# Kernel tuning notes

Measured on AMD Instinct MI355X. Metric: run time of the kernel, lower is better.

The kernel has to match this reference:

```python
import jax, jax.numpy as jnp
import numpy as np

BS = 512          # number of nodes (batch)
EMBED = 256       # embed_dim
NHEAD = 8
HDIM = EMBED // NHEAD
E = BS * BS       # fully-connected intra-batch graph


def _xavier(key, shape):
    lim = float(np.sqrt(6.0 / (shape[0] + shape[1])))
    return jax.random.uniform(key, shape, jnp.float32, -lim, lim)


def setup_inputs() -> dict:
    key = jax.random.key(0)
    ks = jax.random.split(key, 6)
    feats = jax.random.normal(ks[0], (BS, EMBED), jnp.float32)
    # edges sorted by destination c, exactly BS edges per destination
    dst = jnp.repeat(jnp.arange(BS), BS)   # c
    src = jnp.tile(jnp.arange(BS), BS)     # r
    edge_index = jnp.stack([src, dst], axis=1).astype(jnp.int32)  # [E, 2], cols (r, c)
    edge_attr = jnp.zeros((E, 1), jnp.float32)  # unused by forward
    return {
        "feats": feats,
        "edge_index": edge_index,
        "edge_attr": edge_attr,
        "Wq": _xavier(ks[1], (EMBED, EMBED)), "bq": jnp.zeros((EMBED,), jnp.float32),
        "Wk": _xavier(ks[2], (EMBED, EMBED)), "bk": jnp.zeros((EMBED,), jnp.float32),
        "Wv": _xavier(ks[3], (EMBED, EMBED)), "bv": jnp.zeros((EMBED,), jnp.float32),
        "Wo": _xavier(ks[4], (EMBED, EMBED)), "bo": jnp.zeros((EMBED,), jnp.float32),
    }


def reference(feats, edge_index, edge_attr, Wq, bq, Wk, bk, Wv, bv, Wo, bo):
    bs = feats.shape[0]
    scale = 1.0 / np.sqrt(HDIM)
    # QKV projections (torch Linear: x @ W.T + b), split heads -> [h, n, d]
    q = (feats @ Wq.T + bq).reshape(bs, NHEAD, HDIM).transpose(1, 0, 2)
    k = (feats @ Wk.T + bk).reshape(bs, NHEAD, HDIM).transpose(1, 0, 2)
    v = (feats @ Wv.T + bv).reshape(bs, NHEAD, HDIM).transpose(1, 0, 2)
    r, c = edge_index[:, 0], edge_index[:, 1]
    qe = q[:, c, :]   # [h, E, d] query of destination node
    ke = k[:, r, :]   # [h, E, d] key of source node
    ve = v[:, r, :]   # [h, E, d] value of source node
    sim = jnp.einsum('hed,hed->eh', qe, ke) * scale   # [E, h]
    # deterministic segment softmax over edges grouped by destination c
    m = jax.ops.segment_max(sim, c, num_segments=bs)  # [n, h]
    p = jnp.exp(sim - m[c])
    s = jax.ops.segment_sum(p, c, num_segments=bs)    # [n, h]
    attn = p / s[c]                                    # [E, h]
    # weight values and scatter-add per destination (aggr='add')
    out_e = attn.T[..., None] * ve                     # [h, E, d]
    out_e = out_e.transpose(1, 0, 2).reshape(-1, NHEAD * HDIM)  # [E, h*d]
    agg = jax.ops.segment_sum(out_e, c, num_segments=bs)        # [n, embed]
    return agg @ Wo.T + bo
```

## Files before the change

kernel.cpp:

```cpp
#include <hip/hip_runtime.h>

#define BS 512
#define EMBED 256
#define NHEAD 8
#define HDIM 32

typedef __attribute__((ext_vector_type(8))) short short8;
typedef __attribute__((ext_vector_type(4))) float f32x4;

__device__ inline f32x4 mfma16(short8 a, short8 b, f32x4 c) {
    return __builtin_amdgcn_mfma_f32_16x16x32_bf16(a, b, c, 0, 0, 0);
}

__device__ inline unsigned short f2bf(float x) {
    unsigned int u = __float_as_uint(x);
    u += 0x7FFFu + ((u >> 16) & 1u);
    return (unsigned short)(u >> 16);
}
__device__ inline float bf2f(unsigned short h) {
    return __uint_as_float(((unsigned int)h) << 16);
}
__device__ inline void split8(const float* p, short8& hi, short8& lo) {
    float4 a = *(const float4*)p;
    float4 b = *(const float4*)(p + 4);
    float x[8] = {a.x, a.y, a.z, a.w, b.x, b.y, b.z, b.w};
#pragma unroll
    for (int j = 0; j < 8; ++j) {
        unsigned short h = f2bf(x[j]);
        hi[j] = (short)h;
        lo[j] = (short)f2bf(x[j] - bf2f(h));
    }
}

__global__ __launch_bounds__(256) void qkv_fused(
    const float* __restrict__ feats,
    const float* __restrict__ Wq, const float* __restrict__ Wk,
    const float* __restrict__ Wv,
    const float* __restrict__ bq, const float* __restrict__ bk,
    const float* __restrict__ bv,
    unsigned short* __restrict__ Qhi, unsigned short* __restrict__ Qlo,
    unsigned short* __restrict__ Khi, unsigned short* __restrict__ Klo,
    unsigned short* __restrict__ Vthi, unsigned short* __restrict__ Vtlo,
    float* __restrict__ OUT)
{
    const int gidx = blockIdx.x * 256 + threadIdx.x;
    if (gidx < 32768) {
        float4 z = {0.f, 0.f, 0.f, 0.f};
        ((float4*)OUT)[gidx] = z;
    }

    const int wave = blockIdx.x * 4 + (threadIdx.x >> 6);
    const int l = threadIdx.x & 63;
    const int r = l & 15, g = l >> 4;
    const int nt = wave % 48, mt = wave / 48;
    const int m0 = mt * 16, n0 = nt * 16;
    const int seg = n0 >> 8;
    const int nn = n0 & 255;
    const float* W = (seg == 0) ? Wq : (seg == 1) ? Wk : Wv;
    const float* bias = (seg == 0) ? bq : (seg == 1) ? bk : bv;

    const float* arow = feats + (m0 + r) * EMBED;
    const float* brow = W + (nn + r) * EMBED;

    f32x4 acc = {0.f, 0.f, 0.f, 0.f};
#pragma unroll
    for (int kb = 0; kb < 8; ++kb) {
        const int k0 = kb * 32 + g * 8;
        short8 ah, al, bh, bl;
        split8(arow + k0, ah, al);
        split8(brow + k0, bh, bl);
        acc = mfma16(ah, bh, acc);
        acc = mfma16(ah, bl, acc);
        acc = mfma16(al, bh, acc);
    }
    const float bb = bias[nn + r];

    if (seg < 2) {
        unsigned short* Dhi = seg ? Khi : Qhi;
        unsigned short* Dlo = seg ? Klo : Qlo;
#pragma unroll
        for (int r4 = 0; r4 < 4; ++r4) {
            const int i = m0 + g * 4 + r4;
            const int c = nn + r;
            float v = acc[r4] + bb;
            unsigned short hh = f2bf(v);
            Dhi[i * EMBED + c] = hh;
            Dlo[i * EMBED + c] = f2bf(v - bf2f(hh));
        }
    } else {
        const int c = nn + r;
        const int i0 = m0 + g * 4;
        ushort4 ph, pl;
        float v0 = acc[0] + bb, v1 = acc[1] + bb;
        float v2 = acc[2] + bb, v3 = acc[3] + bb;
        ph.x = f2bf(v0); ph.y = f2bf(v1); ph.z = f2bf(v2); ph.w = f2bf(v3);
        pl.x = f2bf(v0 - bf2f(ph.x)); pl.y = f2bf(v1 - bf2f(ph.y));
        pl.z = f2bf(v2 - bf2f(ph.z)); pl.w = f2bf(v3 - bf2f(ph.w));
        *(ushort4*)(Vthi + c * BS + i0) = ph;
        *(ushort4*)(Vtlo + c * BS + i0) = pl;
    }
}

__global__ __launch_bounds__(512) void attn_out(
    const unsigned short* __restrict__ Qhi, const unsigned short* __restrict__ Qlo,
    const unsigned short* __restrict__ Khi, const unsigned short* __restrict__ Klo,
    const unsigned short* __restrict__ Vthi, const unsigned short* __restrict__ Vtlo,
    const float* __restrict__ Wo, const float* __restrict__ bo,
    float* __restrict__ OUT)
{
    const int qt = blockIdx.x >> 3;
    const int h = blockIdx.x & 7;
    const int q0 = qt * 16;
    const int tid = threadIdx.x;
    const int w = tid >> 6, l = tid & 63;
    const int r = l & 15, g = l >> 4;

    __shared__ unsigned short Psm[16 * 512];
    __shared__ float Opart[8][2][256];
    __shared__ float Rpart[8][16];
    __shared__ float Agg[16][36];
    char* Pb = (char*)Psm;

    const short8 qhi = *(const short8*)(Qhi + (q0 + r) * EMBED + h * HDIM + g * 8);
    const short8 qlo = *(const short8*)(Qlo + (q0 + r) * EMBED + h * HDIM + g * 8);

    const float cs = 0.17677669529663687f;
    float rs[4] = {0.f, 0.f, 0.f, 0.f};

#pragma unroll
    for (int kt = 0; kt < 4; ++kt) {
        const int krow = w * 64 + kt * 16 + r;
        short8 kh = *(const short8*)(Khi + krow * EMBED + h * HDIM + g * 8);
        short8 kl = *(const short8*)(Klo + krow * EMBED + h * HDIM + g * 8);
        f32x4 acc = {0.f, 0.f, 0.f, 0.f};
        acc = mfma16(qhi, kh, acc);
        acc = mfma16(qhi, kl, acc);
        acc = mfma16(qlo, kh, acc);
#pragma unroll
        for (int r4 = 0; r4 < 4; ++r4) {
            float p = __expf(acc[r4] * cs);
            rs[r4] += p;
            const int q = g * 4 + r4;
            const int bofs = q * 1024 + ((krow * 2) ^ ((q & 7) << 4));
            *(unsigned short*)(Pb + bofs) = f2bf(p);
        }
    }
#pragma unroll
    for (int off = 1; off < 16; off <<= 1) {
#pragma unroll
        for (int r4 = 0; r4 < 4; ++r4) rs[r4] += __shfl_xor(rs[r4], off);
    }
    if (r == 0) {
#pragma unroll
        for (int r4 = 0; r4 < 4; ++r4) Rpart[w][g * 4 + r4] = rs[r4];
    }

    f32x4 o0 = {0.f, 0.f, 0.f, 0.f}, o1 = {0.f, 0.f, 0.f, 0.f};
    const unsigned short* V0h = Vthi + (h * HDIM + r) * BS;
    const unsigned short* V0l = Vtlo + (h * HDIM + r) * BS;
    const unsigned short* V1h = V0h + 16 * BS;
    const unsigned short* V1l = V0l + 16 * BS;
#pragma unroll
    for (int kc = 0; kc < 2; ++kc) {
        const int kb = w * 64 + kc * 32 + g * 8;
        const int bofs = r * 1024 + ((kb * 2) ^ ((r & 7) << 4));
        short8 pa = *(const short8*)(Pb + bofs);
        o0 = mfma16(pa, *(const short8*)(V0h + kb), o0);
        o0 = mfma16(pa, *(const short8*)(V0l + kb), o0);
        o1 = mfma16(pa, *(const short8*)(V1h + kb), o1);
        o1 = mfma16(pa, *(const short8*)(V1l + kb), o1);
    }
    ((f32x4*)&Opart[w][0][0])[l] = o0;
    ((f32x4*)&Opart[w][1][0])[l] = o1;
    __syncthreads();

    if (w < 2) {
        f32x4 o = ((f32x4*)&Opart[0][w][0])[l];
#pragma unroll
        for (int p = 1; p < 8; ++p) {
            f32x4 t = ((f32x4*)&Opart[p][w][0])[l];
            o[0] += t[0]; o[1] += t[1]; o[2] += t[2]; o[3] += t[3];
        }
#pragma unroll
        for (int r4 = 0; r4 < 4; ++r4) {
            const int q = g * 4 + r4;
            float rt = Rpart[0][q];
#pragma unroll
            for (int p = 1; p < 8; ++p) rt += Rpart[p][q];
            Agg[q][w * 16 + r] = o[r4] / rt;
        }
    }
    __syncthreads();

    short8 ah, al;
    split8(&Agg[r][g * 8], ah, al);
#pragma unroll
    for (int nsub = 0; nsub < 2; ++nsub) {
        const int j0 = w * 32 + nsub * 16;
        short8 bh, bl;
        split8(Wo + (j0 + r) * EMBED + h * HDIM + g * 8, bh, bl);
        f32x4 a = {0.f, 0.f, 0.f, 0.f};
        a = mfma16(ah, bh, a);
        a = mfma16(ah, bl, a);
        a = mfma16(al, bh, a);
#pragma unroll
        for (int r4 = 0; r4 < 4; ++r4) {
            const int row = q0 + g * 4 + r4;
            const int col = j0 + r;
            float v = a[r4];
            if (h == 0) v += bo[col];
            atomicAdd(&OUT[row * EMBED + col], v);
        }
    }
}

extern "C" void kernel_launch(void* const* d_in, const int* in_sizes, int n_in,
                              void* d_out, int out_size, void* d_ws, size_t ws_size,
                              hipStream_t stream) {
    const float* feats = (const float*)d_in[0];
    const float* Wq = (const float*)d_in[3];
    const float* bq = (const float*)d_in[4];
    const float* Wk = (const float*)d_in[5];
    const float* bk = (const float*)d_in[6];
    const float* Wv = (const float*)d_in[7];
    const float* bv = (const float*)d_in[8];
    const float* Wo = (const float*)d_in[9];
    const float* bo = (const float*)d_in[10];
    float* out = (float*)d_out;

    unsigned short* ws = (unsigned short*)d_ws;
    const size_t NE = (size_t)BS * EMBED;
    unsigned short* Qhi  = ws;
    unsigned short* Qlo  = Qhi + NE;
    unsigned short* Khi  = Qlo + NE;
    unsigned short* Klo  = Khi + NE;
    unsigned short* Vthi = Klo + NE;
    unsigned short* Vtlo = Vthi + NE;

    qkv_fused<<<384, 256, 0, stream>>>(feats, Wq, Wk, Wv, bq, bk, bv,
                                       Qhi, Qlo, Khi, Klo, Vthi, Vtlo, out);
    attn_out<<<256, 512, 0, stream>>>(Qhi, Qlo, Khi, Klo, Vthi, Vtlo,
                                      Wo, bo, out);
}
```

Baseline: 26.15 us.

## Give each block all heads per query tile, dropping atomics and output zeroing

The attention kernel now gives each block a 16-query tile. Each wave owns one head and streams all 512 keys in 64-key chunks, so the softmax sum and P·V stay in registers. The 16×256 aggregate is then projected through Wo inside the block and written directly, which removes the atomicAdd reduction and the output-zeroing pass. Wo is pre-split into bf16 hi/lo once in the QKV kernel, and that kernel uses 32×32 wave tiles for more operand reuse. The cost is far fewer blocks (32 attention, 96 QKV), which leaves most compute units idle and lengthens the serial work per wave.

```diff
diff --git a/kernel.cpp b/kernel.cpp
--- a/kernel.cpp
+++ b/kernel.cpp
@@ -35,69 +35,94 @@
 __global__ __launch_bounds__(256) void qkv_fused(
     const float* __restrict__ feats,
     const float* __restrict__ Wq, const float* __restrict__ Wk,
-    const float* __restrict__ Wv,
+    const float* __restrict__ Wv, const float* __restrict__ Wo,
     const float* __restrict__ bq, const float* __restrict__ bk,
     const float* __restrict__ bv,
     unsigned short* __restrict__ Qhi, unsigned short* __restrict__ Qlo,
     unsigned short* __restrict__ Khi, unsigned short* __restrict__ Klo,
     unsigned short* __restrict__ Vthi, unsigned short* __restrict__ Vtlo,
-    float* __restrict__ OUT)
+    unsigned short* __restrict__ Wohi, unsigned short* __restrict__ Wolo)
 {
     const int gidx = blockIdx.x * 256 + threadIdx.x;
-    if (gidx < 32768) {
-        float4 z = {0.f, 0.f, 0.f, 0.f};
-        ((float4*)OUT)[gidx] = z;
+    if (gidx < 16384) {
+        float4 v = ((const float4*)Wo)[gidx];
+        ushort4 ph, pl;
+        ph.x = f2bf(v.x); pl.x = f2bf(v.x - bf2f(ph.x));
+        ph.y = f2bf(v.y); pl.y = f2bf(v.y - bf2f(ph.y));
+        ph.z = f2bf(v.z); pl.z = f2bf(v.z - bf2f(ph.z));
+        ph.w = f2bf(v.w); pl.w = f2bf(v.w - bf2f(ph.w));
+        ((ushort4*)Wohi)[gidx] = ph;
+        ((ushort4*)Wolo)[gidx] = pl;
     }
 
     const int wave = blockIdx.x * 4 + (threadIdx.x >> 6);
     const int l = threadIdx.x & 63;
     const int r = l & 15, g = l >> 4;
-    const int nt = wave % 48, mt = wave / 48;
-    const int m0 = mt * 16, n0 = nt * 16;
+    const int nt = wave % 24, mt = wave / 24;
+    const int m0 = mt * 32, n0 = nt * 32;
     const int seg = n0 >> 8;
     const int nn = n0 & 255;
     const float* W = (seg == 0) ? Wq : (seg == 1) ? Wk : Wv;
     const float* bias = (seg == 0) ? bq : (seg == 1) ? bk : bv;
 
-    const float* arow = feats + (m0 + r) * EMBED;
-    const float* brow = W + (nn + r) * EMBED;
-
-    f32x4 acc = {0.f, 0.f, 0.f, 0.f};
+    const float* a0 = feats + (m0 + r) * EMBED;
+    const float* a1 = a0 + 16 * EMBED;
+    const float* b0 = W + (nn + r) * EMBED;
+    const float* b1 = b0 + 16 * EMBED;
+
+    f32x4 acc00 = {0,0,0,0}, acc01 = {0,0,0,0}, acc10 = {0,0,0,0}, acc11 = {0,0,0,0};
 #pragma unroll
     for (int kb = 0; kb < 8; ++kb) {
         const int k0 = kb * 32 + g * 8;
-        short8 ah, al, bh, bl;
-        split8(arow + k0, ah, al);
-        split8(brow + k0, bh, bl);
-        acc = mfma16(ah, bh, acc);
-        acc = mfma16(ah, bl, acc);
-        acc = mfma16(al, bh, acc);
-    }
-    const float bb = bias[nn + r];
-
-    if (seg < 2) {
-        unsigned short* Dhi = seg ? Khi : Qhi;
-        unsigned short* Dlo = seg ? Klo : Qlo;
-#pragma unroll
-        for (int r4 = 0; r4 < 4; ++r4) {
-            const int i = m0 + g * 4 + r4;
-            const int c = nn + r;
-            float v = acc[r4] + bb;
-            unsigned short hh = f2bf(v);
-            Dhi[i * EMBED + c] = hh;
-            Dlo[i * EMBED + c] = f2bf(v - bf2f(hh));
-        }
-    } else {
-        const int c = nn + r;
-        const int i0 = m0 + g * 4;
-        ushort4 ph, pl;
-        float v0 = acc[0] + bb, v1 = acc[1] + bb;
-        float v2 = acc[2] + bb, v3 = acc[3] + bb;
-        ph.x = f2bf(v0); ph.y = f2bf(v1); ph.z = f2bf(v2); ph.w = f2bf(v3);
-        pl.x = f2bf(v0 - bf2f(ph.x)); pl.y = f2bf(v1 - bf2f(ph.y));
-        pl.z = f2bf(v2 - bf2f(ph.z)); pl.w = f2bf(v3 - bf2f(ph.w));
-        *(ushort4*)(Vthi + c * BS + i0) = ph;
-        *(ushort4*)(Vtlo + c * BS + i0) = pl;
+        short8 A0h, A0l, A1h, A1l, B0h, B0l, B1h, B1l;
+        split8(a0 + k0, A0h, A0l);
+        split8(a1 + k0, A1h, A1l);
+        split8(b0 + k0, B0h, B0l);
+        split8(b1 + k0, B1h, B1l);
+        acc00 = mfma16(A0h, B0h, acc00);
+        acc01 = mfma16(A0h, B1h, acc01);
+        acc10 = mfma16(A1h, B0h, acc10);
+        acc11 = mfma16(A1h, B1h, acc11);
+        acc00 = mfma16(A0h, B0l, acc00);
+        acc01 = mfma16(A0h, B1l, acc01);
+        acc10 = mfma16(A1h, B0l, acc10);
+        acc11 = mfma16(A1h, B1l, acc11);
+        acc00 = mfma16(A0l, B0h, acc00);
+        acc01 = mfma16(A0l, B1h, acc01);
+        acc10 = mfma16(A1l, B0h, acc10);
+        acc11 = mfma16(A1l, B1h, acc11);
+    }
+
+#pragma unroll
+    for (int ti = 0; ti < 2; ++ti) {
+#pragma unroll
+        for (int tj = 0; tj < 2; ++tj) {
+            f32x4 a = (ti == 0) ? (tj == 0 ? acc00 : acc01)
+                                : (tj == 0 ? acc10 : acc11);
+            const int cn = nn + tj * 16 + r;
+            const float bb = bias[cn];
+            if (seg < 2) {
+                unsigned short* Dhi = seg ? Khi : Qhi;
+                unsigned short* Dlo = seg ? Klo : Qlo;
+#pragma unroll
+                for (int r4 = 0; r4 < 4; ++r4) {
+                    const int i = m0 + ti * 16 + g * 4 + r4;
+                    float v = a[r4] + bb;
+                    unsigned short hh = f2bf(v);
+                    Dhi[i * EMBED + cn] = hh;
+                    Dlo[i * EMBED + cn] = f2bf(v - bf2f(hh));
+                }
+            } else {
+                const int i0 = m0 + ti * 16 + g * 4;
+                ushort4 ph, pl;
+                float v0 = a[0] + bb, v1 = a[1] + bb, v2 = a[2] + bb, v3 = a[3] + bb;
+                ph.x = f2bf(v0); ph.y = f2bf(v1); ph.z = f2bf(v2); ph.w = f2bf(v3);
+                pl.x = f2bf(v0 - bf2f(ph.x)); pl.y = f2bf(v1 - bf2f(ph.y));
+                pl.z = f2bf(v2 - bf2f(ph.z)); pl.w = f2bf(v3 - bf2f(ph.w));
+                *(ushort4*)(Vthi + cn * BS + i0) = ph;
+                *(ushort4*)(Vtlo + cn * BS + i0) = pl;
+            }
+        }
     }
 }
 
@@ -105,111 +130,108 @@
     const unsigned short* __restrict__ Qhi, const unsigned short* __restrict__ Qlo,
     const unsigned short* __restrict__ Khi, const unsigned short* __restrict__ Klo,
     const unsigned short* __restrict__ Vthi, const unsigned short* __restrict__ Vtlo,
-    const float* __restrict__ Wo, const float* __restrict__ bo,
-    float* __restrict__ OUT)
+    const unsigned short* __restrict__ Wohi, const unsigned short* __restrict__ Wolo,
+    const float* __restrict__ bo, float* __restrict__ OUT)
 {
-    const int qt = blockIdx.x >> 3;
-    const int h = blockIdx.x & 7;
-    const int q0 = qt * 16;
+    const int q0 = blockIdx.x * 16;
     const int tid = threadIdx.x;
     const int w = tid >> 6, l = tid & 63;
     const int r = l & 15, g = l >> 4;
 
-    __shared__ unsigned short Psm[16 * 512];
-    __shared__ float Opart[8][2][256];
-    __shared__ float Rpart[8][16];
-    __shared__ float Agg[16][36];
-    char* Pb = (char*)Psm;
-
-    const short8 qhi = *(const short8*)(Qhi + (q0 + r) * EMBED + h * HDIM + g * 8);
-    const short8 qlo = *(const short8*)(Qlo + (q0 + r) * EMBED + h * HDIM + g * 8);
+    __shared__ unsigned short Psm[8][16 * 64];
+    __shared__ float Agg[16][260];
+    char* Pb = (char*)&Psm[w][0];
+
+    const short8 qhi = *(const short8*)(Qhi + (q0 + r) * EMBED + w * HDIM + g * 8);
+    const short8 qlo = *(const short8*)(Qlo + (q0 + r) * EMBED + w * HDIM + g * 8);
 
     const float cs = 0.17677669529663687f;
     float rs[4] = {0.f, 0.f, 0.f, 0.f};
-
-#pragma unroll
-    for (int kt = 0; kt < 4; ++kt) {
-        const int krow = w * 64 + kt * 16 + r;
-        short8 kh = *(const short8*)(Khi + krow * EMBED + h * HDIM + g * 8);
-        short8 kl = *(const short8*)(Klo + krow * EMBED + h * HDIM + g * 8);
-        f32x4 acc = {0.f, 0.f, 0.f, 0.f};
-        acc = mfma16(qhi, kh, acc);
-        acc = mfma16(qhi, kl, acc);
-        acc = mfma16(qlo, kh, acc);
-#pragma unroll
-        for (int r4 = 0; r4 < 4; ++r4) {
-            float p = __expf(acc[r4] * cs);
-            rs[r4] += p;
-            const int q = g * 4 + r4;
-            const int bofs = q * 1024 + ((krow * 2) ^ ((q & 7) << 4));
-            *(unsigned short*)(Pb + bofs) = f2bf(p);
-        }
-    }
-#pragma unroll
-    for (int off = 1; off < 16; off <<= 1) {
-#pragma unroll
-        for (int r4 = 0; r4 < 4; ++r4) rs[r4] += __shfl_xor(rs[r4], off);
-    }
-    if (r == 0) {
-#pragma unroll
-        for (int r4 = 0; r4 < 4; ++r4) Rpart[w][g * 4 + r4] = rs[r4];
-    }
-
     f32x4 o0 = {0.f, 0.f, 0.f, 0.f}, o1 = {0.f, 0.f, 0.f, 0.f};
-    const unsigned short* V0h = Vthi + (h * HDIM + r) * BS;
-    const unsigned short* V0l = Vtlo + (h * HDIM + r) * BS;
+
+    const unsigned short* V0h = Vthi + (w * HDIM + r) * BS;
+    const unsigned short* V0l = Vtlo + (w * HDIM + r) * BS;
     const unsigned short* V1h = V0h + 16 * BS;
     const unsigned short* V1l = V0l + 16 * BS;
-#pragma unroll
-    for (int kc = 0; kc < 2; ++kc) {
-        const int kb = w * 64 + kc * 32 + g * 8;
-        const int bofs = r * 1024 + ((kb * 2) ^ ((r & 7) << 4));
-        short8 pa = *(const short8*)(Pb + bofs);
-        o0 = mfma16(pa, *(const short8*)(V0h + kb), o0);
-        o0 = mfma16(pa, *(const short8*)(V0l + kb), o0);
-        o1 = mfma16(pa, *(const short8*)(V1h + kb), o1);
-        o1 = mfma16(pa, *(const short8*)(V1l + kb), o1);
-    }
-    ((f32x4*)&Opart[w][0][0])[l] = o0;
-    ((f32x4*)&Opart[w][1][0])[l] = o1;
+
+#pragma unroll
+    for (int t = 0; t < 8; ++t) {
+        const int t0 = t * 64;
+#pragma unroll
+        for (int kt = 0; kt < 4; ++kt) {
+            const int krow = t0 + kt * 16 + r;
+            short8 kh = *(const short8*)(Khi + krow * EMBED + w * HDIM + g * 8);
+            short8 kl = *(const short8*)(Klo + krow * EMBED + w * HDIM + g * 8);
+            f32x4 acc = {0.f, 0.f, 0.f, 0.f};
+            acc = mfma16(qhi, kh, acc);
+            acc = mfma16(qhi, kl, acc);
+            acc = mfma16(qlo, kh, acc);
+#pragma unroll
+            for (int r4 = 0; r4 < 4; ++r4) {
+                float p = __expf(acc[r4] * cs);
+                rs[r4] += p;
+                const int q = g * 4 + r4;
+                const int kk = kt * 16 + r;
+                const int bofs = q * 128 + ((kk * 2) ^ ((q & 7) << 4));
+                *(unsigned short*)(Pb + bofs) = f2bf(p);
+            }
+        }
+#pragma unroll
+        for (int kc = 0; kc < 2; ++kc) {
+            const int kk = kc * 32 + g * 8;
+            const int kb = t0 + kk;
+            const int bofs = r * 128 + ((kk * 2) ^ ((r & 7) << 4));
+            short8 pa = *(const short8*)(Pb + bofs);
+            o0 = mfma16(pa, *(const short8*)(V0h + kb), o0);
+            o0 = mfma16(pa, *(const short8*)(V0l + kb), o0);
+            o1 = mfma16(pa, *(const short8*)(V1h + kb), o1);
+            o1 = mfma16(pa, *(const short8*)(V1l + kb), o1);
+        }
+    }
+#pragma unroll
+    for (int off = 1; off < 16; off <<= 1) {
+#pragma unroll
+        for (int r4 = 0; r4 < 4; ++r4) rs[r4] += __shfl_xor(rs[r4], off);
+    }
+#pragma unroll
+    for (int r4 = 0; r4 < 4; ++r4) {
+        const int q = g * 4 + r4;
+        const float inv = 1.0f / rs[r4];
+        Agg[q][w * 32 + r] = o0[r4] * inv;
+        Agg[q][w * 32 + 16 + r] = o1[r4] * inv;
+    }
     __syncthreads();
 
-    if (w < 2) {
-        f32x4 o = ((f32x4*)&Opart[0][w][0])[l];
-#pragma unroll
-        for (int p = 1; p < 8; ++p) {
-            f32x4 t = ((f32x4*)&Opart[p][w][0])[l];
-            o[0] += t[0]; o[1] += t[1]; o[2] += t[2]; o[3] += t[3];
-        }
+    f32x4 p0 = {0.f, 0.f, 0.f, 0.f}, p1 = {0.f, 0.f, 0.f, 0.f};
+#pragma unroll
+    for (int kb = 0; kb < 8; ++kb) {
+        short8 ah, al;
+        split8(&Agg[r][kb * 32 + g * 8], ah, al);
+        {
+            const int j0 = w * 32;
+            short8 bh = *(const short8*)(Wohi + (j0 + r) * EMBED + kb * 32 + g * 8);
+            short8 bl = *(const short8*)(Wolo + (j0 + r) * EMBED + kb * 32 + g * 8);
+            p0 = mfma16(ah, bh, p0);
+            p0 = mfma16(ah, bl, p0);
+            p0 = mfma16(al, bh, p0);
+        }
+        {
+            const int j0 = w * 32 + 16;
+            short8 bh = *(const short8*)(Wohi + (j0 + r) * EMBED + kb * 32 + g * 8);
+            short8 bl = *(const short8*)(Wolo + (j0 + r) * EMBED + kb * 32 + g * 8);
+            p1 = mfma16(ah, bh, p1);
+            p1 = mfma16(ah, bl, p1);
+            p1 = mfma16(al, bh, p1);
+        }
+    }
+#pragma unroll
+    for (int nsub = 0; nsub < 2; ++nsub) {
+        const f32x4 a = nsub ? p1 : p0;
+        const int j0 = w * 32 + nsub * 16;
+        const float bb = bo[j0 + r];
 #pragma unroll
         for (int r4 = 0; r4 < 4; ++r4) {
-            const int q = g * 4 + r4;
-            float rt = Rpart[0][q];
-#pragma unroll
-            for (int p = 1; p < 8; ++p) rt += Rpart[p][q];
-            Agg[q][w * 16 + r] = o[r4] / rt;
-        }
-    }
-    __syncthreads();
-
-    short8 ah, al;
-    split8(&Agg[r][g * 8], ah, al);
-#pragma unroll
-    for (int nsub = 0; nsub < 2; ++nsub) {
-        const int j0 = w * 32 + nsub * 16;
-        short8 bh, bl;
-        split8(Wo + (j0 + r) * EMBED + h * HDIM + g * 8, bh, bl);
-        f32x4 a = {0.f, 0.f, 0.f, 0.f};
-        a = mfma16(ah, bh, a);
-        a = mfma16(ah, bl, a);
-        a = mfma16(al, bh, a);
-#pragma unroll
-        for (int r4 = 0; r4 < 4; ++r4) {
-            const int row = q0 + g * 4 + r4;
-            const int col = j0 + r;
-            float v = a[r4];
-            if (h == 0) v += bo[col];
-            atomicAdd(&OUT[row * EMBED + col], v);
+            OUT[(q0 + g * 4 + r4) * EMBED + j0 + r] = a[r4] + bb;
         }
     }
 }
@@ -230,15 +252,19 @@
 
     unsigned short* ws = (unsigned short*)d_ws;
     const size_t NE = (size_t)BS * EMBED;
+    const size_t WO = (size_t)EMBED * EMBED;
     unsigned short* Qhi  = ws;
     unsigned short* Qlo  = Qhi + NE;
     unsigned short* Khi  = Qlo + NE;
     unsigned short* Klo  = Khi + NE;
     unsigned short* Vthi = Klo + NE;
     unsigned short* Vtlo = Vthi + NE;
-
-    qkv_fused<<<384, 256, 0, stream>>>(feats, Wq, Wk, Wv, bq, bk, bv,
-                                       Qhi, Qlo, Khi, Klo, Vthi, Vtlo, out);
-    attn_out<<<256, 512, 0, stream>>>(Qhi, Qlo, Khi, Klo, Vthi, Vtlo,
-                                      Wo, bo, out);
-}
+    unsigned short* Wohi = Vtlo + NE;
+    unsigned short* Wolo = Wohi + WO;
+
+    qkv_fused<<<96, 256, 0, stream>>>(feats, Wq, Wk, Wv, Wo, bq, bk, bv,
+                                      Qhi, Qlo, Khi, Klo, Vthi, Vtlo,
+                                      Wohi, Wolo);
+    attn_out<<<32, 512, 0, stream>>>(Qhi, Qlo, Khi, Klo, Vthi, Vtlo,
+                                     Wohi, Wolo, bo, out);
+}
```

New measurement: 56.69 us. 2.17x slower.
